# Kernel optimization log

Measured on AMD Instinct MI355X. Metric: run time of the kernel, lower is better.

The kernel has to match this reference:

```python
import math
import jax, jax.numpy as jnp
import numpy as np

B, S, D, H, DH, R, V = 8, 1024, 1024, 8, 512, 36, 32002  # DH = d_model//2, HD = h*DH = 4096
HD = H * DH
LN_EPS = 1e-5


def setup_inputs() -> dict:
    key = jax.random.key(0)
    ks = jax.random.split(key, 16)

    def n(k, shp, std=0.02):
        return jax.random.normal(k, shp, jnp.float32) * std

    pre_words = jax.random.randint(ks[0], (B, S), 0, V)
    img_features = jax.random.normal(ks[1], (B, R, D), jnp.float32)
    exp_embed = n(ks[2], (V, D)).at[0].set(0.0)  # padding_idx=0
    # id2visual table: sparse nonneg rows over 36 regions; zero rows -> textual tokens
    id2vis = (jax.random.uniform(ks[3], (V, R)) < 0.05).astype(jnp.float32)
    # stacked params for 2 transformer layers; weights stored (in, out) so y = x @ W + b
    wq = n(ks[4], (2, D, HD)); bq = jnp.zeros((2, HD), jnp.float32)
    wk = n(ks[5], (2, D, HD)); bk = jnp.zeros((2, HD), jnp.float32)
    wv = n(ks[6], (2, D, HD)); bv = jnp.zeros((2, HD), jnp.float32)
    wo = n(ks[7], (2, HD, D)); bo = jnp.zeros((2, D), jnp.float32)
    w1 = n(ks[8], (2, D, D)); b1 = jnp.zeros((2, D), jnp.float32)
    w2 = n(ks[9], (2, D, D)); b2 = jnp.zeros((2, D), jnp.float32)
    ln1_g = jnp.ones((2, D), jnp.float32); ln1_b = jnp.zeros((2, D), jnp.float32)
    ln2_g = jnp.ones((2, D), jnp.float32); ln2_b = jnp.zeros((2, D), jnp.float32)
    return dict(pre_words=pre_words, img_features=img_features, exp_embed=exp_embed,
                id2vis=id2vis, wq=wq, bq=bq, wk=wk, bk=bk, wv=wv, bv=bv, wo=wo, bo=bo,
                w1=w1, b1=b1, w2=w2, b2=b2, ln1_g=ln1_g, ln1_b=ln1_b, ln2_g=ln2_g, ln2_b=ln2_b)


def _layer_norm(x, g, b):
    m = x.mean(-1, keepdims=True)
    v = ((x - m) ** 2).mean(-1, keepdims=True)
    return (x - m) / jnp.sqrt(v + LN_EPS) * g + b


def _softmax_one(x):
    # shifted-denominator softmax: exp(x - max) / (1 + sum exp(x - max))
    x = x - x.max(-1, keepdims=True)
    e = jnp.exp(x)
    return e / (1.0 + e.sum(-1, keepdims=True))


def reference(pre_words, img_features, exp_embed, id2vis, wq, bq, wk, bk, wv, bv,
              wo, bo, w1, b1, w2, b2, ln1_g, ln1_b, ln2_g, ln2_b):
    # token embedding: textual (masked to 0 where a visual row exists) + visual bmm
    te = exp_embed[pre_words]                       # (B,S,D)
    vids = id2vis[pre_words]                        # (B,S,R)
    word_mask = vids.sum(-1, keepdims=True) != 0    # (B,S,1)
    ve = jnp.einsum('bsr,brd->bsd', vids, img_features)
    x = jnp.where(word_mask, 0.0, te) + ve          # (B,S,D)

    scale = 1.0 / math.sqrt(DH)
    for i in range(2):  # two structurally identical transformer layers
        h = _layer_norm(x, ln1_g[i], ln1_b[i])
        q = (h @ wq[i] + bq[i]).reshape(B, S, H, DH).transpose(0, 2, 1, 3)
        k = (h @ wk[i] + bk[i]).reshape(B, S, H, DH).transpose(0, 2, 1, 3)
        v = (h @ wv[i] + bv[i]).reshape(B, S, H, DH).transpose(0, 2, 1, 3)
        attn = _softmax_one(jnp.einsum('bhqd,bhkd->bhqk', q, k) * scale)  # (B,H,S,S)
        o = jnp.einsum('bhqk,bhkd->bhqd', attn, v)
        o = o.transpose(0, 2, 1, 3).reshape(B, S, HD)
        x = x + (o @ wo[i] + bo[i])
        f = _layer_norm(x, ln2_g[i], ln2_b[i])
        f = jax.nn.gelu(f @ w1[i] + b1[i], approximate=False) @ w2[i] + b2[i]
        x = x + f
    return x
```

## Files before the change

### kernel.cpp

```cpp
#include <hip/hip_runtime.h>


using u16 = unsigned short;
typedef __attribute__((ext_vector_type(8))) short bf16x8;
typedef __attribute__((ext_vector_type(4))) float f32x4;

__device__ __forceinline__ float b2f(u16 u) {
  union { unsigned int i; float f; } v; v.i = ((unsigned int)u) << 16; return v.f;
}
__device__ __forceinline__ u16 f2b(float f) {
  union { float f; unsigned int i; } v; v.f = f;
  unsigned int i = v.i;
  return (u16)((i + 0x7FFFu + ((i >> 16) & 1u)) >> 16);
}
__device__ __forceinline__ float gelu_f(float x) {
  return 0.5f * x * (1.f + erff(x * 0.70710678118654752f));
}
__device__ __forceinline__ void async16(void* lds, const void* g) {
  __builtin_amdgcn_global_load_lds((const __attribute__((address_space(1))) void*)g,
                                   (__attribute__((address_space(3))) void*)lds, 16, 0, 0);
}
__device__ __forceinline__ void storeC(float* p, float v) { *p = v; }
__device__ __forceinline__ void storeC(u16* p, float v) { *p = f2b(v); }

__global__ __launch_bounds__(256) void embed_k(
    const int* __restrict__ words, const float* __restrict__ img,
    const float* __restrict__ emb, const float* __restrict__ id2v,
    float* __restrict__ x)
{
  __shared__ float vs[36];
  int tok = blockIdx.x, b = tok >> 10, t = threadIdx.x;
  int wd = words[tok];
  if (t < 36) vs[t] = id2v[(size_t)wd * 36 + t];
  __syncthreads();
  bool any = false;
#pragma unroll
  for (int r = 0; r < 36; ++r) any = any || (vs[r] != 0.f);
#pragma unroll
  for (int i = 0; i < 4; ++i) {
    int d = t + (i << 8);
    float acc = 0.f;
    for (int r = 0; r < 36; ++r) {
      float vv = vs[r];
      if (vv != 0.f) acc += vv * img[((size_t)(b * 36 + r) << 10) + d];
    }
    float te = any ? 0.f : emb[((size_t)wd << 10) + d];
    x[((size_t)tok << 10) + d] = te + acc;
  }
}

__global__ __launch_bounds__(256) void ln_k(
    const float* __restrict__ x, u16* __restrict__ out,
    const float* __restrict__ g, const float* __restrict__ bb)
{
  __shared__ float red[4];
  int row = blockIdx.x, t = threadIdx.x;
  const float* xr = x + ((size_t)row << 10);
  float v[4], s = 0.f;
#pragma unroll
  for (int i = 0; i < 4; ++i) { v[i] = xr[t + (i << 8)]; s += v[i]; }
#pragma unroll
  for (int o = 32; o; o >>= 1) s += __shfl_xor(s, o, 64);
  if ((t & 63) == 0) red[t >> 6] = s;
  __syncthreads();
  s = red[0] + red[1] + red[2] + red[3];
  float mean = s * 0.0009765625f;
  float q = 0.f;
#pragma unroll
  for (int i = 0; i < 4; ++i) { float d = v[i] - mean; q += d * d; }
  __syncthreads();
#pragma unroll
  for (int o = 32; o; o >>= 1) q += __shfl_xor(q, o, 64);
  if ((t & 63) == 0) red[t >> 6] = q;
  __syncthreads();
  q = red[0] + red[1] + red[2] + red[3];
  float rstd = rsqrtf(q * 0.0009765625f + 1e-5f);
  u16* orow = out + ((size_t)row << 10);
#pragma unroll
  for (int i = 0; i < 4; ++i) {
    int d = t + (i << 8);
    orow[d] = f2b((v[i] - mean) * rstd * g[d] + bb[d]);
  }
}

__global__ __launch_bounds__(256) void sm_k(const float* __restrict__ S, u16* __restrict__ P)
{
  __shared__ float red[4];
  size_t row = blockIdx.x;
  int t = threadIdx.x;
  const float* sr = S + (row << 10);
  float v[4], m = -3.0e38f;
#pragma unroll
  for (int i = 0; i < 4; ++i) { v[i] = sr[t + (i << 8)]; m = fmaxf(m, v[i]); }
#pragma unroll
  for (int o = 32; o; o >>= 1) m = fmaxf(m, __shfl_xor(m, o, 64));
  if ((t & 63) == 0) red[t >> 6] = m;
  __syncthreads();
  m = fmaxf(fmaxf(red[0], red[1]), fmaxf(red[2], red[3]));
  float e[4], s = 0.f;
#pragma unroll
  for (int i = 0; i < 4; ++i) { e[i] = __expf(v[i] - m); s += e[i]; }
  __syncthreads();
#pragma unroll
  for (int o = 32; o; o >>= 1) s += __shfl_xor(s, o, 64);
  if ((t & 63) == 0) red[t >> 6] = s;
  __syncthreads();
  s = red[0] + red[1] + red[2] + red[3];
  float inv = 1.f / (1.f + s);
  u16* pr = P + (row << 10);
#pragma unroll
  for (int i = 0; i < 4; ++i) pr[t + (i << 8)] = f2b(e[i] * inv);
}

__global__ __launch_bounds__(256) void tr_k(
    const float* __restrict__ src, u16* __restrict__ dst, int ls, int ld)
{
  __shared__ u16 tile[64][65];
  int c0 = blockIdx.x << 6, r0 = blockIdx.y << 6;
  int tx = threadIdx.x & 63, ty0 = threadIdx.x >> 6;
#pragma unroll
  for (int i = 0; i < 16; ++i) {
    int ty = (ty0 << 4) + i;
    tile[ty][tx] = f2b(src[(size_t)(r0 + ty) * ls + (c0 + tx)]);
  }
  __syncthreads();
#pragma unroll
  for (int i = 0; i < 16; ++i) {
    int ty = (ty0 << 4) + i;
    dst[(size_t)(c0 + ty) * ld + (r0 + tx)] = tile[tx][ty];
  }
}

template <typename CT, int ACT, int BIAS, int RESID>
__global__ __launch_bounds__(256, 2) void gemm_bt(
    const u16* __restrict__ A, const u16* __restrict__ Bt,
    CT* __restrict__ C, const float* __restrict__ bias,
    const float* __restrict__ resid,
    int M, int N, int K, int lda, int ldb, int ldc, float scale,
    int zbase, int zdiv, int ga, int gb, int gc,
    long long aS1, long long aS2, long long bS1, long long bS2,
    long long cS1, long long cS2)
{
  __shared__ u16 lA[128 * 32];
  __shared__ u16 lB[128 * 32];
  long long lz = blockIdx.z;
  long long gz = zbase + lz;
  long long zA = ga ? gz : lz, zB = gb ? gz : lz, zC = gc ? gz : lz;
  size_t aOff = (size_t)((zA / zdiv) * aS1 + (zA % zdiv) * aS2);
  size_t bOff = (size_t)((zB / zdiv) * bS1 + (zB % zdiv) * bS2);
  size_t cOff = (size_t)((zC / zdiv) * cS1 + (zC % zdiv) * cS2);
  const int m0 = blockIdx.y << 7, n0 = blockIdx.x << 7;
  const int tid = threadIdx.x, lane = tid & 63, w = tid >> 6;
  const int wr = (w >> 1) << 6, wc = (w & 1) << 6;
  const int srow = lane >> 2, skoff = (lane & 3) << 3;
  const int kk = (lane >> 4) << 3, fr = lane & 15;

  f32x4 acc[4][4];
#pragma unroll
  for (int mi = 0; mi < 4; ++mi)
#pragma unroll
    for (int ni = 0; ni < 4; ++ni) acc[mi][ni] = 0.f;

  for (int k0 = 0; k0 < K; k0 += 32) {
#pragma unroll
    for (int i = 0; i < 2; ++i) {
      const int rb = (w << 5) + (i << 4);
      async16(&lA[rb << 5], A + aOff + (size_t)(m0 + rb + srow) * lda + (k0 + skoff));
      async16(&lB[rb << 5], Bt + bOff + (size_t)(n0 + rb + srow) * ldb + (k0 + skoff));
    }
    __syncthreads();
    bf16x8 af[4], bfr[4];
#pragma unroll
    for (int mi = 0; mi < 4; ++mi)
      af[mi] = *(const bf16x8*)&lA[((wr + (mi << 4) + fr) << 5) + kk];
#pragma unroll
    for (int ni = 0; ni < 4; ++ni)
      bfr[ni] = *(const bf16x8*)&lB[((wc + (ni << 4) + fr) << 5) + kk];
#pragma unroll
    for (int mi = 0; mi < 4; ++mi)
#pragma unroll
      for (int ni = 0; ni < 4; ++ni)
        acc[mi][ni] = __builtin_amdgcn_mfma_f32_16x16x32_bf16(af[mi], bfr[ni], acc[mi][ni], 0, 0, 0);
    __syncthreads();
  }

  const int r4 = (lane >> 4) << 2, cc = lane & 15;
#pragma unroll
  for (int mi = 0; mi < 4; ++mi) {
#pragma unroll
    for (int ni = 0; ni < 4; ++ni) {
      const int col = n0 + wc + (ni << 4) + cc;
      float bcol = 0.f;
      if (BIAS == 1) bcol = bias[col];
#pragma unroll
      for (int j = 0; j < 4; ++j) {
        const int row = m0 + wr + (mi << 4) + r4 + j;
        float v = acc[mi][ni][j] * scale + bcol;
        if (BIAS == 2) v += bias[row];
        if (ACT == 1) v = gelu_f(v);
        const size_t idx = cOff + (size_t)row * ldc + col;
        if (RESID) v += resid[idx];
        storeC(&C[idx], v);
      }
    }
  }
}

extern "C" void kernel_launch(void* const* d_in, const int* in_sizes, int n_in,
                              void* d_out, int out_size, void* d_ws, size_t ws_size,
                              hipStream_t stream)
{
  (void)in_sizes; (void)n_in; (void)out_size;
  const int*   pre_words = (const int*)d_in[0];
  const float* img  = (const float*)d_in[1];
  const float* emb  = (const float*)d_in[2];
  const float* id2v = (const float*)d_in[3];
  const float* wq = (const float*)d_in[4];  const float* bq = (const float*)d_in[5];
  const float* wk = (const float*)d_in[6];  const float* bk = (const float*)d_in[7];
  const float* wv = (const float*)d_in[8];  const float* bv = (const float*)d_in[9];
  const float* wo = (const float*)d_in[10]; const float* bo = (const float*)d_in[11];
  const float* w1 = (const float*)d_in[12]; const float* b1 = (const float*)d_in[13];
  const float* w2 = (const float*)d_in[14]; const float* b2 = (const float*)d_in[15];
  const float* ln1g = (const float*)d_in[16]; const float* ln1b = (const float*)d_in[17];
  const float* ln2g = (const float*)d_in[18]; const float* ln2b = (const float*)d_in[19];

  const size_t FIXED = 88080384 + (size_t)(1 << 16);
  int g = 1;
  for (int c = 8; c >= 1; c >>= 1)
    if (FIXED + (size_t)c * 33554432 + 6291456 <= ws_size) { g = c; break; }
  int nc = 1;
  for (int c = 8 * g; c >= 1; c >>= 1)
    if (FIXED + (size_t)g * 33554432 + (size_t)c * 6291456 <= ws_size) { nc = c; break; }

  char* p = (char*)d_ws;
  auto alloc = [&](size_t bytes) -> void* {
    void* r = (void*)p; p += (bytes + 255) & ~(size_t)255; return r;
  };
  float* x  = (float*)alloc((size_t)8192 * 1024 * 4);
  u16* h    = (u16*)alloc((size_t)8192 * 1024 * 2);
  u16* Qg   = (u16*)alloc((size_t)g * 1024 * 4096 * 2);
  u16* Og   = (u16*)alloc((size_t)g * 1024 * 4096 * 2);
  u16* ff   = Qg;
  u16* Kg   = (u16*)alloc((size_t)g * 1024 * 4096 * 2);
  u16* Vtg  = (u16*)alloc((size_t)g * 4096 * 1024 * 2);
  u16* wqt  = (u16*)alloc((size_t)4096 * 1024 * 2);
  u16* wkt  = (u16*)alloc((size_t)4096 * 1024 * 2);
  u16* wvt  = (u16*)alloc((size_t)4096 * 1024 * 2);
  u16* wot  = (u16*)alloc((size_t)1024 * 4096 * 2);
  u16* w1t  = (u16*)alloc((size_t)1024 * 1024 * 2);
  u16* w2t  = (u16*)alloc((size_t)1024 * 1024 * 2);
  float* Sc = (float*)alloc((size_t)nc << 22);
  u16*  Pp  = (u16*)alloc((size_t)nc << 21);

  embed_k<<<8192, 256, 0, stream>>>(pre_words, img, emb, id2v, x);

  const float qk_scale = 0.044194173824159216f;
  for (int L = 0; L < 2; ++L) {
    const float* WQ = wq + (size_t)L * 1024 * 4096;
    const float* WK = wk + (size_t)L * 1024 * 4096;
    const float* WV = wv + (size_t)L * 1024 * 4096;
    const float* WO = wo + (size_t)L * 4096 * 1024;
    const float* W1 = w1 + (size_t)L * 1024 * 1024;
    const float* W2 = w2 + (size_t)L * 1024 * 1024;

    tr_k<<<dim3(64, 16), 256, 0, stream>>>(WQ, wqt, 4096, 1024);
    tr_k<<<dim3(64, 16), 256, 0, stream>>>(WK, wkt, 4096, 1024);
    tr_k<<<dim3(64, 16), 256, 0, stream>>>(WV, wvt, 4096, 1024);
    tr_k<<<dim3(16, 64), 256, 0, stream>>>(WO, wot, 1024, 4096);
    tr_k<<<dim3(16, 16), 256, 0, stream>>>(W1, w1t, 1024, 1024);
    tr_k<<<dim3(16, 16), 256, 0, stream>>>(W2, w2t, 1024, 1024);

    ln_k<<<8192, 256, 0, stream>>>(x, h, ln1g + L * 1024, ln1b + L * 1024);

    for (int g0 = 0; g0 < 8; g0 += g) {
      const u16* hg = h + (size_t)g0 * 1048576;
      const int Mg = 1024 * g;
      gemm_bt<u16, 0, 1, 0><<<dim3(32, Mg >> 7), 256, 0, stream>>>(
          hg, wqt, Qg, bq + (size_t)L * 4096, nullptr,
          Mg, 4096, 1024, 1024, 1024, 4096, 1.f,
          0, 1, 0, 0, 0, 0, 0, 0, 0, 0, 0);
      gemm_bt<u16, 0, 1, 0><<<dim3(32, Mg >> 7), 256, 0, stream>>>(
          hg, wkt, Kg, bk + (size_t)L * 4096, nullptr,
          Mg, 4096, 1024, 1024, 1024, 4096, 1.f,
          0, 1, 0, 0, 0, 0, 0, 0, 0, 0, 0);
      gemm_bt<u16, 0, 2, 0><<<dim3(8, 32, g), 256, 0, stream>>>(
          wvt, h, Vtg, bv + (size_t)L * 4096, nullptr,
          4096, 1024, 1024, 1024, 1024, 1024, 1.f,
          g0, 1, 0, 1, 0, 0, 0, 1048576LL, 0, 4194304LL, 0);
      for (int c0 = 0; c0 < 8 * g; c0 += nc) {
        gemm_bt<float, 0, 0, 0><<<dim3(8, 8, nc), 256, 0, stream>>>(
            Qg, Kg, Sc, nullptr, nullptr,
            1024, 1024, 512, 4096, 4096, 1024, qk_scale,
            c0, 8, 1, 1, 0,
            4194304LL, 512LL, 4194304LL, 512LL, 8388608LL, 1048576LL);
        sm_k<<<nc << 10, 256, 0, stream>>>(Sc, Pp);
        gemm_bt<u16, 0, 0, 0><<<dim3(4, 8, nc), 256, 0, stream>>>(
            Pp, Vtg, Og, nullptr, nullptr,
            1024, 512, 1024, 1024, 1024, 4096, 1.f,
            c0, 8, 0, 1, 1,
            8388608LL, 1048576LL, 4194304LL, 524288LL, 4194304LL, 512LL);
      }
      gemm_bt<float, 0, 1, 1><<<dim3(8, Mg >> 7), 256, 0, stream>>>(
          Og, wot, x + (size_t)g0 * 1048576, bo + (size_t)L * 1024,
          x + (size_t)g0 * 1048576,
          Mg, 1024, 4096, 4096, 4096, 1024, 1.f,
          0, 1, 0, 0, 0, 0, 0, 0, 0, 0, 0);
    }

    ln_k<<<8192, 256, 0, stream>>>(x, h, ln2g + L * 1024, ln2b + L * 1024);

    gemm_bt<u16, 1, 1, 0><<<dim3(8, 64), 256, 0, stream>>>(
        h, w1t, ff, b1 + (size_t)L * 1024, nullptr,
        8192, 1024, 1024, 1024, 1024, 1024, 1.f,
        0, 1, 0, 0, 0, 0, 0, 0, 0, 0, 0);
    float* cdst = (L == 1) ? (float*)d_out : x;
    gemm_bt<float, 0, 1, 1><<<dim3(8, 64), 256, 0, stream>>>(
        ff, w2t, cdst, b2 + (size_t)L * 1024, x,
        8192, 1024, 1024, 1024, 1024, 1024, 1.f,
        0, 1, 0, 0, 0, 0, 0, 0, 0, 0, 0);
  }
}
```

Measured before the change: 1.801 ms.

## Add 256x256-tile double-buffered GEMM kernel for QKV and attention matmuls

Adds a new 512-thread GEMM kernel with 256x256 output tiles and K-step 64. It double-buffers LDS through async global-to-LDS loads and uses XOR-swizzled reads feeding 16x16x32 bf16 MFMAs. The Q/K/V projections and both attention batched GEMMs now use it to raise arithmetic intensity and cut global traffic per FLOP. The attention chunk count is also capped at 32. The larger tiles mean fewer blocks and one block per CU with heavy register use (128 accumulator floats per thread), so occupancy and tail effects are the risk.

```diff
diff --git a/kernel.cpp b/kernel.cpp
--- a/kernel.cpp
+++ b/kernel.cpp
@@ -128,6 +128,101 @@
   for (int i = 0; i < 16; ++i) {
     int ty = (ty0 << 4) + i;
     dst[(size_t)(c0 + ty) * ld + (r0 + tx)] = tile[tx][ty];
+  }
+}
+
+template <typename CT, int ACT, int BIAS, int RESID>
+__global__ __launch_bounds__(512, 1) void gemm256(
+    const u16* __restrict__ A, const u16* __restrict__ Bt,
+    CT* __restrict__ C, const float* __restrict__ bias,
+    const float* __restrict__ resid,
+    int M, int N, int K, int lda, int ldb, int ldc, float scale,
+    int zbase, int zdiv, int ga, int gb, int gc,
+    long long aS1, long long aS2, long long bS1, long long bS2,
+    long long cS1, long long cS2)
+{
+  __shared__ u16 lds[2][2][256 * 64];
+  long long lz = blockIdx.z;
+  long long gz = zbase + lz;
+  long long zA = ga ? gz : lz, zB = gb ? gz : lz, zC = gc ? gz : lz;
+  size_t aOff = (size_t)((zA / zdiv) * aS1 + (zA % zdiv) * aS2);
+  size_t bOff = (size_t)((zB / zdiv) * bS1 + (zB % zdiv) * bS2);
+  size_t cOff = (size_t)((zC / zdiv) * cS1 + (zC % zdiv) * cS2);
+  const int m0 = blockIdx.y << 8, n0 = blockIdx.x << 8;
+  const int tid = threadIdx.x, lane = tid & 63, w = tid >> 6;
+  const int wm = w >> 2, wn = w & 3;
+  const int srow8 = lane >> 3;
+  const int schunk = (lane & 7) ^ srow8;
+  const int fr = lane & 15, hi = lane >> 4;
+
+  f32x4 acc[8][4];
+#pragma unroll
+  for (int mi = 0; mi < 8; ++mi)
+#pragma unroll
+    for (int ni = 0; ni < 4; ++ni) acc[mi][ni] = 0.f;
+
+  const u16* Ab = A + aOff;
+  const u16* Bb = Bt + bOff;
+
+  auto STAGE = [&](int buf, int k0) {
+#pragma unroll
+    for (int r = 0; r < 4; ++r) {
+      const int rbase = (r << 6) + (w << 3);
+      async16(&lds[buf][0][rbase << 6],
+              Ab + (size_t)(m0 + rbase + srow8) * lda + (k0 + (schunk << 3)));
+      async16(&lds[buf][1][rbase << 6],
+              Bb + (size_t)(n0 + rbase + srow8) * ldb + (k0 + (schunk << 3)));
+    }
+  };
+
+  STAGE(0, 0);
+  __syncthreads();
+  const int nt = K >> 6;
+  for (int t = 0; t < nt; ++t) {
+    const int cur = t & 1;
+    if (t + 1 < nt) STAGE(cur ^ 1, (t + 1) << 6);
+#pragma unroll
+    for (int ks = 0; ks < 2; ++ks) {
+      const int q = (ks << 2) + hi;
+      bf16x8 a8[8], b8[4];
+#pragma unroll
+      for (int mi = 0; mi < 8; ++mi) {
+        const int R = (wm << 7) + (mi << 4) + fr;
+        a8[mi] = *(const bf16x8*)&lds[cur][0][(R << 6) + ((q ^ (R & 7)) << 3)];
+      }
+#pragma unroll
+      for (int ni = 0; ni < 4; ++ni) {
+        const int R = (wn << 6) + (ni << 4) + fr;
+        b8[ni] = *(const bf16x8*)&lds[cur][1][(R << 6) + ((q ^ (R & 7)) << 3)];
+      }
+#pragma unroll
+      for (int mi = 0; mi < 8; ++mi)
+#pragma unroll
+        for (int ni = 0; ni < 4; ++ni)
+          acc[mi][ni] = __builtin_amdgcn_mfma_f32_16x16x32_bf16(a8[mi], b8[ni], acc[mi][ni], 0, 0, 0);
+    }
+    __syncthreads();
+  }
+
+  const int r4 = hi << 2, cc = fr;
+#pragma unroll
+  for (int mi = 0; mi < 8; ++mi) {
+#pragma unroll
+    for (int ni = 0; ni < 4; ++ni) {
+      const int col = n0 + (wn << 6) + (ni << 4) + cc;
+      float bcol = 0.f;
+      if (BIAS == 1) bcol = bias[col];
+#pragma unroll
+      for (int j = 0; j < 4; ++j) {
+        const int row = m0 + (wm << 7) + (mi << 4) + r4 + j;
+        float v = acc[mi][ni][j] * scale + bcol;
+        if (BIAS == 2) v += bias[row];
+        if (ACT == 1) v = gelu_f(v);
+        const size_t idx = cOff + (size_t)row * ldc + col;
+        if (RESID) v += resid[idx];
+        storeC(&C[idx], v);
+      }
+    }
   }
 }
 
@@ -229,7 +324,8 @@
   for (int c = 8; c >= 1; c >>= 1)
     if (FIXED + (size_t)c * 33554432 + 6291456 <= ws_size) { g = c; break; }
   int nc = 1;
-  for (int c = 8 * g; c >= 1; c >>= 1)
+  int ncmax = 8 * g > 32 ? 32 : 8 * g;
+  for (int c = ncmax; c >= 1; c >>= 1)
     if (FIXED + (size_t)g * 33554432 + (size_t)c * 6291456 <= ws_size) { nc = c; break; }
 
   char* p = (char*)d_ws;
@@ -275,26 +371,26 @@
     for (int g0 = 0; g0 < 8; g0 += g) {
       const u16* hg = h + (size_t)g0 * 1048576;
       const int Mg = 1024 * g;
-      gemm_bt<u16, 0, 1, 0><<<dim3(32, Mg >> 7), 256, 0, stream>>>(
+      gemm256<u16, 0, 1, 0><<<dim3(16, Mg >> 8), 512, 0, stream>>>(
           hg, wqt, Qg, bq + (size_t)L * 4096, nullptr,
           Mg, 4096, 1024, 1024, 1024, 4096, 1.f,
           0, 1, 0, 0, 0, 0, 0, 0, 0, 0, 0);
-      gemm_bt<u16, 0, 1, 0><<<dim3(32, Mg >> 7), 256, 0, stream>>>(
+      gemm256<u16, 0, 1, 0><<<dim3(16, Mg >> 8), 512, 0, stream>>>(
           hg, wkt, Kg, bk + (size_t)L * 4096, nullptr,
           Mg, 4096, 1024, 1024, 1024, 4096, 1.f,
           0, 1, 0, 0, 0, 0, 0, 0, 0, 0, 0);
-      gemm_bt<u16, 0, 2, 0><<<dim3(8, 32, g), 256, 0, stream>>>(
+      gemm256<u16, 0, 2, 0><<<dim3(4, 16, g), 512, 0, stream>>>(
           wvt, h, Vtg, bv + (size_t)L * 4096, nullptr,
           4096, 1024, 1024, 1024, 1024, 1024, 1.f,
           g0, 1, 0, 1, 0, 0, 0, 1048576LL, 0, 4194304LL, 0);
       for (int c0 = 0; c0 < 8 * g; c0 += nc) {
-        gemm_bt<float, 0, 0, 0><<<dim3(8, 8, nc), 256, 0, stream>>>(
+        gemm256<float, 0, 0, 0><<<dim3(4, 4, nc), 512, 0, stream>>>(
             Qg, Kg, Sc, nullptr, nullptr,
             1024, 1024, 512, 4096, 4096, 1024, qk_scale,
             c0, 8, 1, 1, 0,
             4194304LL, 512LL, 4194304LL, 512LL, 8388608LL, 1048576LL);
         sm_k<<<nc << 10, 256, 0, stream>>>(Sc, Pp);
-        gemm_bt<u16, 0, 0, 0><<<dim3(4, 8, nc), 256, 0, stream>>>(
+        gemm256<u16, 0, 0, 0><<<dim3(2, 4, nc), 512, 0, stream>>>(
             Pp, Vtg, Og, nullptr, nullptr,
             1024, 512, 1024, 1024, 1024, 4096, 1.f,
             c0, 8, 0, 1, 1,
```

Result: faster. 1.689 ms (-6.2%).

## Deepen GEMM K-tile to 64 with XOR-swizzled LDS and XCD-aware block remap

Applied to the files above, without the earlier changes.

The bf16 MFMA GEMM now stages 64-wide K slices instead of 32, halving the number of barrier pairs per K loop. An XOR swizzle on the 16-byte chunk index removes LDS bank conflicts when fragments are read. Workgroup IDs are remapped so consecutive tiles land on the same XCD for better L2 reuse, and launch bounds ask for 4 waves per SIMD. The attention chunk count is also capped at 32 batches. The trade-off is doubled LDS per block, which could limit occupancy, and more address arithmetic.

```diff
diff --git a/kernel.cpp b/kernel.cpp
--- a/kernel.cpp
+++ b/kernel.cpp
@@ -132,7 +132,7 @@
 }
 
 template <typename CT, int ACT, int BIAS, int RESID>
-__global__ __launch_bounds__(256, 2) void gemm_bt(
+__global__ __launch_bounds__(256, 4) void gemm128(
     const u16* __restrict__ A, const u16* __restrict__ Bt,
     CT* __restrict__ C, const float* __restrict__ bias,
     const float* __restrict__ resid,
@@ -141,19 +141,27 @@
     long long aS1, long long aS2, long long bS1, long long bS2,
     long long cS1, long long cS2)
 {
-  __shared__ u16 lA[128 * 32];
-  __shared__ u16 lB[128 * 32];
+  __shared__ u16 lA[128 * 64];
+  __shared__ u16 lB[128 * 64];
+  const int nwg = gridDim.x * gridDim.y;
+  const int id = blockIdx.y * gridDim.x + blockIdx.x;
+  const int qq = nwg >> 3, rr8 = nwg & 7;
+  const int xcd = id & 7, off = id >> 3;
+  const int swz = (xcd < rr8 ? xcd * (qq + 1) : rr8 * (qq + 1) + (xcd - rr8) * qq) + off;
+  const int bx = swz % gridDim.x, by = swz / gridDim.x;
+
   long long lz = blockIdx.z;
   long long gz = zbase + lz;
   long long zA = ga ? gz : lz, zB = gb ? gz : lz, zC = gc ? gz : lz;
   size_t aOff = (size_t)((zA / zdiv) * aS1 + (zA % zdiv) * aS2);
   size_t bOff = (size_t)((zB / zdiv) * bS1 + (zB % zdiv) * bS2);
   size_t cOff = (size_t)((zC / zdiv) * cS1 + (zC % zdiv) * cS2);
-  const int m0 = blockIdx.y << 7, n0 = blockIdx.x << 7;
+  const int m0 = by << 7, n0 = bx << 7;
   const int tid = threadIdx.x, lane = tid & 63, w = tid >> 6;
-  const int wr = (w >> 1) << 6, wc = (w & 1) << 6;
-  const int srow = lane >> 2, skoff = (lane & 3) << 3;
-  const int kk = (lane >> 4) << 3, fr = lane & 15;
+  const int wm = w >> 1, wn = w & 1;
+  const int srow8 = lane >> 3;
+  const int schunk = (lane & 7) ^ srow8;
+  const int fr = lane & 15, hi = lane >> 4;
 
   f32x4 acc[4][4];
 #pragma unroll
@@ -161,40 +169,51 @@
 #pragma unroll
     for (int ni = 0; ni < 4; ++ni) acc[mi][ni] = 0.f;
 
-  for (int k0 = 0; k0 < K; k0 += 32) {
-#pragma unroll
-    for (int i = 0; i < 2; ++i) {
-      const int rb = (w << 5) + (i << 4);
-      async16(&lA[rb << 5], A + aOff + (size_t)(m0 + rb + srow) * lda + (k0 + skoff));
-      async16(&lB[rb << 5], Bt + bOff + (size_t)(n0 + rb + srow) * ldb + (k0 + skoff));
+  const u16* Ab = A + aOff;
+  const u16* Bb = Bt + bOff;
+
+  for (int k0 = 0; k0 < K; k0 += 64) {
+#pragma unroll
+    for (int s = 0; s < 4; ++s) {
+      const int rb = (s << 5) + (w << 3);
+      async16(&lA[rb << 6], Ab + (size_t)(m0 + rb + srow8) * lda + (k0 + (schunk << 3)));
+      async16(&lB[rb << 6], Bb + (size_t)(n0 + rb + srow8) * ldb + (k0 + (schunk << 3)));
     }
     __syncthreads();
-    bf16x8 af[4], bfr[4];
-#pragma unroll
-    for (int mi = 0; mi < 4; ++mi)
-      af[mi] = *(const bf16x8*)&lA[((wr + (mi << 4) + fr) << 5) + kk];
-#pragma unroll
-    for (int ni = 0; ni < 4; ++ni)
-      bfr[ni] = *(const bf16x8*)&lB[((wc + (ni << 4) + fr) << 5) + kk];
-#pragma unroll
-    for (int mi = 0; mi < 4; ++mi)
-#pragma unroll
-      for (int ni = 0; ni < 4; ++ni)
-        acc[mi][ni] = __builtin_amdgcn_mfma_f32_16x16x32_bf16(af[mi], bfr[ni], acc[mi][ni], 0, 0, 0);
+#pragma unroll
+    for (int ks = 0; ks < 2; ++ks) {
+      const int q = (ks << 2) + hi;
+      bf16x8 a8[4], b8[4];
+#pragma unroll
+      for (int mi = 0; mi < 4; ++mi) {
+        const int R = (wm << 6) + (mi << 4) + fr;
+        a8[mi] = *(const bf16x8*)&lA[(R << 6) + ((q ^ (R & 7)) << 3)];
+      }
+#pragma unroll
+      for (int ni = 0; ni < 4; ++ni) {
+        const int R = (wn << 6) + (ni << 4) + fr;
+        b8[ni] = *(const bf16x8*)&lB[(R << 6) + ((q ^ (R & 7)) << 3)];
+      }
+#pragma unroll
+      for (int mi = 0; mi < 4; ++mi)
+#pragma unroll
+        for (int ni = 0; ni < 4; ++ni)
+          acc[mi][ni] = __builtin_amdgcn_mfma_f32_16x16x32_bf16(a8[mi], b8[ni], acc[mi][ni], 0, 0, 0);
+    }
     __syncthreads();
   }
 
-  const int r4 = (lane >> 4) << 2, cc = lane & 15;
+  const int r4 = hi << 2, cc = fr;
 #pragma unroll
   for (int mi = 0; mi < 4; ++mi) {
 #pragma unroll
     for (int ni = 0; ni < 4; ++ni) {
-      const int col = n0 + wc + (ni << 4) + cc;
+      const int col = n0 + (wn << 6) + (ni << 4) + cc;
       float bcol = 0.f;
       if (BIAS == 1) bcol = bias[col];
 #pragma unroll
       for (int j = 0; j < 4; ++j) {
-        const int row = m0 + wr + (mi << 4) + r4 + j;
+        const int row = m0 + (wm << 6) + (mi << 4) + r4 + j;
         float v = acc[mi][ni][j] * scale + bcol;
         if (BIAS == 2) v += bias[row];
         if (ACT == 1) v = gelu_f(v);
@@ -229,7 +248,8 @@
   for (int c = 8; c >= 1; c >>= 1)
     if (FIXED + (size_t)c * 33554432 + 6291456 <= ws_size) { g = c; break; }
   int nc = 1;
-  for (int c = 8 * g; c >= 1; c >>= 1)
+  int ncmax = 8 * g > 32 ? 32 : 8 * g;
+  for (int c = ncmax; c >= 1; c >>= 1)
     if (FIXED + (size_t)g * 33554432 + (size_t)c * 6291456 <= ws_size) { nc = c; break; }
 
   char* p = (char*)d_ws;
@@ -275,32 +295,32 @@
     for (int g0 = 0; g0 < 8; g0 += g) {
       const u16* hg = h + (size_t)g0 * 1048576;
       const int Mg = 1024 * g;
-      gemm_bt<u16, 0, 1, 0><<<dim3(32, Mg >> 7), 256, 0, stream>>>(
+      gemm128<u16, 0, 1, 0><<<dim3(32, Mg >> 7), 256, 0, stream>>>(
           hg, wqt, Qg, bq + (size_t)L * 4096, nullptr,
           Mg, 4096, 1024, 1024, 1024, 4096, 1.f,
           0, 1, 0, 0, 0, 0, 0, 0, 0, 0, 0);
-      gemm_bt<u16, 0, 1, 0><<<dim3(32, Mg >> 7), 256, 0, stream>>>(
+      gemm128<u16, 0, 1, 0><<<dim3(32, Mg >> 7), 256, 0, stream>>>(
           hg, wkt, Kg, bk + (size_t)L * 4096, nullptr,
           Mg, 4096, 1024, 1024, 1024, 4096, 1.f,
           0, 1, 0, 0, 0, 0, 0, 0, 0, 0, 0);
-      gemm_bt<u16, 0, 2, 0><<<dim3(8, 32, g), 256, 0, stream>>>(
+      gemm128<u16, 0, 2, 0><<<dim3(8, 32, g), 256, 0, stream>>>(
           wvt, h, Vtg, bv + (size_t)L * 4096, nullptr,
           4096, 1024, 1024, 1024, 1024, 1024, 1.f,
           g0, 1, 0, 1, 0, 0, 0, 1048576LL, 0, 4194304LL, 0);
       for (int c0 = 0; c0 < 8 * g; c0 += nc) {
-        gemm_bt<float, 0, 0, 0><<<dim3(8, 8, nc), 256, 0, stream>>>(
+        gemm128<float, 0, 0, 0><<<dim3(8, 8, nc), 256, 0, stream>>>(
             Qg, Kg, Sc, nullptr, nullptr,
             1024, 1024, 512, 4096, 4096, 1024, qk_scale,
             c0, 8, 1, 1, 0,
             4194304LL, 512LL, 4194304LL, 512LL, 8388608LL, 1048576LL);
         sm_k<<<nc << 10, 256, 0, stream>>>(Sc, Pp);
-        gemm_bt<u16, 0, 0, 0><<<dim3(4, 8, nc), 256, 0, stream>>>(
+        gemm128<u16, 0, 0, 0><<<dim3(4, 8, nc), 256, 0, stream>>>(
             Pp, Vtg, Og, nullptr, nullptr,
             1024, 512, 1024, 1024, 1024, 4096, 1.f,
             c0, 8, 0, 1, 1,
             8388608LL, 1048576LL, 4194304LL, 524288LL, 4194304LL, 512LL);
       }
-      gemm_bt<float, 0, 1, 1><<<dim3(8, Mg >> 7), 256, 0, stream>>>(
+      gemm128<float, 0, 1, 1><<<dim3(8, Mg >> 7), 256, 0, stream>>>(
           Og, wot, x + (size_t)g0 * 1048576, bo + (size_t)L * 1024,
           x + (size_t)g0 * 1048576,
           Mg, 1024, 4096, 4096, 4096, 1024, 1.f,
@@ -309,12 +329,12 @@
 
     ln_k<<<8192, 256, 0, stream>>>(x, h, ln2g + L * 1024, ln2b + L * 1024);
 
-    gemm_bt<u16, 1, 1, 0><<<dim3(8, 64), 256, 0, stream>>>(
+    gemm128<u16, 1, 1, 0><<<dim3(8, 64), 256, 0, stream>>>(
         h, w1t, ff, b1 + (size_t)L * 1024, nullptr,
         8192, 1024, 1024, 1024, 1024, 1024, 1.f,
         0, 1, 0, 0, 0, 0, 0, 0, 0, 0, 0);
     float* cdst = (L == 1) ? (float*)d_out : x;
-    gemm_bt<float, 0, 1, 1><<<dim3(8, 64), 256, 0, stream>>>(
+    gemm128<float, 0, 1, 1><<<dim3(8, 64), 256, 0, stream>>>(
         ff, w2t, cdst, b2 + (size_t)L * 1024, x,
         8192, 1024, 1024, 1024, 1024, 1024, 1.f,
         0, 1, 0, 0, 0, 0, 0, 0, 0, 0, 0);
```

Result: faster. 1.655 ms (-8.1%).
